# Kernel optimization log

Hardware: AMD Instinct MI355X
Metric: run time of the kernel (lower is better)

## Reference

```python
import jax, jax.numpy as jnp
import numpy as np

HEAD_DIM = 32
N_HEADS = 8
Q_DIM = 128
FF_DIM = 4 * Q_DIM
EPS = 1e-5


def layernorm(x, gamma, beta):
    mu = jnp.mean(x, axis=-1, keepdims=True)
    var = jnp.var(x, axis=-1, keepdims=True)
    return (x - mu) * jax.lax.rsqrt(var + EPS) * gamma + beta


def setup_inputs() -> dict:
    key = jax.random.key(0)
    ks = jax.random.split(key, 20)
    S, B = 1024, 16
    sc_in = 1.0 / np.sqrt(Q_DIM)
    sc_hd = 1.0 / np.sqrt(N_HEADS * HEAD_DIM)
    sc_ff = 1.0 / np.sqrt(FF_DIM)
    return {
        "sequence": jax.random.normal(ks[0], (S, B, Q_DIM), jnp.float32),
        # per-head Q/K/V projections, stacked over heads: [H, Q_dim, head_dim]
        "Wq": jax.random.uniform(ks[1], (N_HEADS, Q_DIM, HEAD_DIM), jnp.float32, -sc_in, sc_in),
        "bq": jax.random.uniform(ks[2], (N_HEADS, HEAD_DIM), jnp.float32, -sc_in, sc_in),
        "Wk": jax.random.uniform(ks[3], (N_HEADS, Q_DIM, HEAD_DIM), jnp.float32, -sc_in, sc_in),
        "bk": jax.random.uniform(ks[4], (N_HEADS, HEAD_DIM), jnp.float32, -sc_in, sc_in),
        "Wv": jax.random.uniform(ks[5], (N_HEADS, Q_DIM, HEAD_DIM), jnp.float32, -sc_in, sc_in),
        "bv": jax.random.uniform(ks[6], (N_HEADS, HEAD_DIM), jnp.float32, -sc_in, sc_in),
        # post_head_linear: [H*head_dim, Q_dim]
        "Wo": jax.random.uniform(ks[7], (N_HEADS * HEAD_DIM, Q_DIM), jnp.float32, -sc_hd, sc_hd),
        "bo": jax.random.uniform(ks[8], (Q_DIM,), jnp.float32, -sc_hd, sc_hd),
        # norm1 (note: original reuses norm1 for both layernorms)
        "gamma1": jnp.ones((Q_DIM,), jnp.float32),
        "beta1": jnp.zeros((Q_DIM,), jnp.float32),
        # FFN: Q_dim -> 4Q -> 4Q -> Q_dim
        "W1": jax.random.uniform(ks[9], (Q_DIM, FF_DIM), jnp.float32, -sc_in, sc_in),
        "b1": jax.random.uniform(ks[10], (FF_DIM,), jnp.float32, -sc_in, sc_in),
        "W2": jax.random.uniform(ks[11], (FF_DIM, FF_DIM), jnp.float32, -sc_ff, sc_ff),
        "b2": jax.random.uniform(ks[12], (FF_DIM,), jnp.float32, -sc_ff, sc_ff),
        "W3": jax.random.uniform(ks[13], (FF_DIM, Q_DIM), jnp.float32, -sc_ff, sc_ff),
        "b3": jax.random.uniform(ks[14], (Q_DIM,), jnp.float32, -sc_ff, sc_ff),
    }


def reference(sequence, Wq, bq, Wk, bk, Wv, bv, Wo, bo, gamma1, beta1, W1, b1, W2, b2, W3, b3):
    # sequence: [S, B, Q_dim] -> batch-first [B, S, Q_dim]
    x = jnp.transpose(sequence, (1, 0, 2))
    # batched per-head projections: [B, H, S, d]
    q = jnp.einsum('bsq,hqd->bhsd', x, Wq) + bq[None, :, None, :]
    k = jnp.einsum('bsq,hqd->bhsd', x, Wk) + bk[None, :, None, :]
    v = jnp.einsum('bsq,hqd->bhsd', x, Wv) + bv[None, :, None, :]
    scores = jnp.einsum('bhsd,bhtd->bhst', q, k) / np.sqrt(HEAD_DIM)
    attn = jax.nn.softmax(scores, axis=-1)
    o = jnp.einsum('bhst,bhtd->bhsd', attn, v)  # [B, H, S, d]
    B, H, S, d = o.shape
    o = jnp.transpose(o, (0, 2, 1, 3)).reshape(B, S, H * d)  # concat heads
    att_outs = o @ Wo + bo
    att_outs = layernorm(x + att_outs, gamma1, beta1)
    h = jax.nn.relu(att_outs @ W1 + b1)
    h = jax.nn.relu(h @ W2 + b2)
    h = h @ W3 + b3
    out = layernorm(att_outs + h, gamma1, beta1)  # original reuses norm1
    return jnp.transpose(out, (1, 0, 2))  # back to [S, B, Q_dim]
```

## Files before the change

kernel.cpp:

```cpp
#include <hip/hip_runtime.h>
#include <hip/hip_bf16.h>

#define S_LEN 1024
#define BATCH 16
#define QD 128
#define NH 8
#define HD 32
#define FF 512
#define NROWS (BATCH * S_LEN)
#define EPS 1e-5f

typedef __attribute__((ext_vector_type(4))) float f32x4;
typedef __attribute__((ext_vector_type(8))) short s16x8;
typedef __attribute__((ext_vector_type(4))) short s16x4;

__device__ __forceinline__ ushort f2bfu(float f) {
    union { float f; unsigned u; } v; v.f = f;
    unsigned r = (v.u + 0x7FFFu + ((v.u >> 16) & 1u)) >> 16;
    return (ushort)r;
}

__device__ __forceinline__ float bf2f(ushort u) {
    union { unsigned u; float f; } v; v.u = ((unsigned)u) << 16;
    return v.f;
}

__device__ __forceinline__ float exp2_fast(float x) {
#if __has_builtin(__builtin_amdgcn_exp2f)
    return __builtin_amdgcn_exp2f(x);
#else
    float r;
    asm("v_exp_f32 %0, %1" : "=v"(r) : "v"(x));
    return r;
#endif
}

__device__ __forceinline__ unsigned pk_bf16(float a, float b) {
    union { __hip_bfloat162 h; unsigned u; } c;
    c.h = __float22bfloat162_rn(make_float2(a, b));
    return c.u;
}

static __device__ __forceinline__ f32x4 mfma16(s16x4 a, s16x4 b, f32x4 c) {
#if __has_builtin(__builtin_amdgcn_mfma_f32_16x16x16bf16_1k)
    return __builtin_amdgcn_mfma_f32_16x16x16bf16_1k(a, b, c, 0, 0, 0);
#else
    asm volatile("v_mfma_f32_16x16x16_bf16 %0, %1, %2, %0" : "+v"(c) : "v"(a), "v"(b));
    return c;
#endif
}

static __device__ __forceinline__ f32x4 mfma32(s16x8 a, s16x8 b, f32x4 c) {
    return __builtin_amdgcn_mfma_f32_16x16x32_bf16(a, b, c, 0, 0, 0);
}

__device__ __forceinline__ void gl_lds16(const void* g, void* l) {
    __builtin_amdgcn_global_load_lds(
        (const __attribute__((address_space(1))) void*)g,
        (__attribute__((address_space(3))) void*)l, 16, 0, 0);
}

template <int K>
__device__ __forceinline__ void gemm_core(
    const ushort* __restrict__ act, const ushort* __restrict__ WTp,
    char* lds, int tok0, f32x4 acc[8]) {
    const int tid = threadIdx.x;
    const int w = tid >> 6, lane = tid & 63;
    const int qi = lane & 15, g = lane >> 4;
    const int r8 = tid >> 3;
    const int csw = (tid & 7) ^ (r8 & 7);
    const int wave_base = w * 1024;
    constexpr int NT = K / 64;

    auto STAGE = [&](int b, int ks) {
        char* buf = lds + b * 24576;
#pragma unroll
        for (int i = 0; i < 4; ++i)
            gl_lds16(WTp + (size_t)(i * 32 + r8) * K + ks + csw * 8,
                     buf + i * 4096 + wave_base);
#pragma unroll
        for (int j = 0; j < 2; ++j)
            gl_lds16(act + (size_t)(tok0 + j * 32 + r8) * K + ks + csw * 8,
                     buf + 16384 + j * 4096 + wave_base);
    };

    STAGE(0, 0);
    int cur = 0;
#pragma unroll 1
    for (int t = 0; t < NT; ++t) {
        if (t < NT - 1) {
            STAGE(cur ^ 1, (t + 1) * 64);
            asm volatile("s_waitcnt vmcnt(6)" ::: "memory");
        } else {
            asm volatile("s_waitcnt vmcnt(0)" ::: "memory");
        }
        __builtin_amdgcn_sched_barrier(0);
        __builtin_amdgcn_s_barrier();
        __builtin_amdgcn_sched_barrier(0);
        const char* A = lds + cur * 24576;
        const char* B = A + 16384;
        const int brow = w * 16 + qi;
        __builtin_amdgcn_s_setprio(1);
#pragma unroll
        for (int kk2 = 0; kk2 < 2; ++kk2) {
            s16x8 bfrag = *(const s16x8*)(B + brow * 128 +
                                          (((kk2 * 4 + g) ^ (brow & 7)) * 16));
#pragma unroll
            for (int f = 0; f < 8; ++f) {
                const int row = qi + 16 * f;
                s16x8 afrag = *(const s16x8*)(A + row * 128 +
                                              (((kk2 * 4 + g) ^ (row & 7)) * 16));
                acc[f] = mfma32(afrag, bfrag, acc[f]);
            }
        }
        __builtin_amdgcn_s_setprio(0);
        __builtin_amdgcn_sched_barrier(0);
        __builtin_amdgcn_s_barrier();
        __builtin_amdgcn_sched_barrier(0);
        cur ^= 1;
    }
}

template <int K>
__device__ __forceinline__ void gemm_core2(
    const ushort* __restrict__ act, const ushort* __restrict__ WTp,
    char* lds, int tok0, f32x4 accA[8], f32x4 accB[8]) {
    const int tid = threadIdx.x;
    const int w = tid >> 6, lane = tid & 63;
    const int qi = lane & 15, g = lane >> 4;
    const int r8 = tid >> 3;
    const int csw = (tid & 7) ^ (r8 & 7);
    const int wave_base = w * 1024;
    constexpr int NT = K / 64;

    auto STAGE = [&](int b, int ks) {
        char* buf = lds + b * 32768;
#pragma unroll
        for (int i = 0; i < 4; ++i)
            gl_lds16(WTp + (size_t)(i * 32 + r8) * K + ks + csw * 8,
                     buf + i * 4096 + wave_base);
#pragma unroll
        for (int j = 0; j < 4; ++j)
            gl_lds16(act + (size_t)(tok0 + j * 32 + r8) * K + ks + csw * 8,
                     buf + 16384 + j * 4096 + wave_base);
    };

    STAGE(0, 0);
    int cur = 0;
#pragma unroll 1
    for (int t = 0; t < NT; ++t) {
        if (t < NT - 1) {
            STAGE(cur ^ 1, (t + 1) * 64);
            asm volatile("s_waitcnt vmcnt(8)" ::: "memory");
        } else {
            asm volatile("s_waitcnt vmcnt(0)" ::: "memory");
        }
        __builtin_amdgcn_sched_barrier(0);
        __builtin_amdgcn_s_barrier();
        __builtin_amdgcn_sched_barrier(0);
        const char* A = lds + cur * 32768;
        const char* Bq = A + 16384;
        const int brow0 = w * 32 + qi;
        const int brow1 = brow0 + 16;
        __builtin_amdgcn_s_setprio(1);
#pragma unroll
        for (int kk2 = 0; kk2 < 2; ++kk2) {
            s16x8 bf0 = *(const s16x8*)(Bq + brow0 * 128 +
                                        (((kk2 * 4 + g) ^ (brow0 & 7)) * 16));
            s16x8 bf1 = *(const s16x8*)(Bq + brow1 * 128 +
                                        (((kk2 * 4 + g) ^ (brow0 & 7)) * 16));
#pragma unroll
            for (int f = 0; f < 8; ++f) {
                const int row = qi + 16 * f;
                s16x8 afrag = *(const s16x8*)(A + row * 128 +
                                              (((kk2 * 4 + g) ^ (row & 7)) * 16));
                accA[f] = mfma32(afrag, bf0, accA[f]);
                accB[f] = mfma32(afrag, bf1, accB[f]);
            }
        }
        __builtin_amdgcn_s_setprio(0);
        __builtin_amdgcn_sched_barrier(0);
        __builtin_amdgcn_s_barrier();
        __builtin_amdgcn_sched_barrier(0);
        cur ^= 1;
    }
}

__global__ __launch_bounds__(256) void prep_all(
    const float* __restrict__ seq, ushort* __restrict__ x_bf,
    const float* __restrict__ Wo, const float* __restrict__ W1,
    const float* __restrict__ W2, const float* __restrict__ W3,
    const float* __restrict__ Wq, const float* __restrict__ Wk,
    const float* __restrict__ Wv,
    ushort* __restrict__ WoT, ushort* __restrict__ W1T,
    ushort* __restrict__ W2T, ushort* __restrict__ W3T,
    ushort* __restrict__ WqkvT) {
    if (blockIdx.x < 2048) {
        int t = blockIdx.x * 256 + threadIdx.x;
        int e4 = t * 4;
        int s = e4 >> 11, b = (e4 >> 7) & 15, c = e4 & 127;
        float4 v = *(const float4*)(seq + e4);
        ushort4 o = {f2bfu(v.x), f2bfu(v.y), f2bfu(v.z), f2bfu(v.w)};
        *(ushort4*)(x_bf + ((size_t)(b * 1024 + s)) * 128 + c) = o;
        return;
    }
    int idx = (blockIdx.x - 2048) * 256 + threadIdx.x;
    if (idx < 32768) {
        int n = idx >> 8, k = idx & 255;
        WoT[n * 256 + k] = f2bfu(Wo[k * 128 + n]);
    } else if (idx < 98304) {
        int i = idx - 32768; int n = i >> 7, k = i & 127;
        W1T[n * 128 + k] = f2bfu(W1[k * 512 + n]);
    } else if (idx < 360448) {
        int i = idx - 98304; int n = i >> 9, k = i & 511;
        W2T[n * 512 + k] = f2bfu(W2[k * 512 + n]);
    } else if (idx < 425984) {
        int i = idx - 360448; int n = i >> 9, k = i & 511;
        W3T[n * 512 + k] = f2bfu(W3[k * 128 + n]);
    } else {
        int i = idx - 425984;
        int n = i >> 7, k = i & 127;
        int p = n >> 8, h = (n >> 5) & 7, d = n & 31;
        const float* W = (p == 0) ? Wq : (p == 1) ? Wk : Wv;
        WqkvT[n * 128 + k] = f2bfu(W[(h * QD + k) * HD + d]);
    }
}

__global__ __launch_bounds__(256) void qkv_mfma(
    const ushort* __restrict__ x_bf, const ushort* __restrict__ WqkvT,
    const float* __restrict__ bq, const float* __restrict__ bk,
    const float* __restrict__ bv,
    ushort* __restrict__ q_bf, ushort* __restrict__ k_bf,
    ushort* __restrict__ vT) {
    __shared__ __align__(16) char lds[2 * 32768];
    const int lane = threadIdx.x & 63;
    const int w = threadIdx.x >> 6;
    const int qi = lane & 15, g = lane >> 4;
    const int tok0 = blockIdx.x * 128;
    const int n0 = blockIdx.y * 128;

    f32x4 accA[8], accB[8];
#pragma unroll
    for (int f = 0; f < 8; ++f) {
        accA[f] = (f32x4){0.f, 0.f, 0.f, 0.f};
        accB[f] = (f32x4){0.f, 0.f, 0.f, 0.f};
    }
    gemm_core2<128>(x_bf, WqkvT + (size_t)n0 * 128, lds, tok0, accA, accB);

    const float SCALE = 0.25503491f;
#define QKV_EPI(ACC, TOK)                                                      \
    do {                                                                       \
        const int b_ = (TOK) >> 10, s_ = (TOK) & 1023;                         \
        if (n0 < 256) {                                                        \
            _Pragma("unroll") for (int f = 0; f < 8; ++f) {                    \
                int n = n0 + 16 * f + 4 * g;                                   \
                int h = (n >> 5) & 7, d = n & 31;                              \
                ushort4 pv = {f2bfu((ACC[f][0] + bq[h * 32 + d + 0]) * SCALE), \
                              f2bfu((ACC[f][1] + bq[h * 32 + d + 1]) * SCALE), \
                              f2bfu((ACC[f][2] + bq[h * 32 + d + 2]) * SCALE), \
                              f2bfu((ACC[f][3] + bq[h * 32 + d + 3]) * SCALE)};\
                *(ushort4*)(q_bf + ((size_t)(b_ * 8 + h) * 1024 + s_) * 32 + d) = pv; \
            }                                                                  \
        } else if (n0 < 512) {                                                 \
            _Pragma("unroll") for (int f = 0; f < 8; ++f) {                    \
                int n = n0 + 16 * f + 4 * g;                                   \
                int h = (n >> 5) & 7, d = n & 31;                              \
                ushort4 pv = {f2bfu(ACC[f][0] + bk[h * 32 + d + 0]),           \
                              f2bfu(ACC[f][1] + bk[h * 32 + d + 1]),           \
                              f2bfu(ACC[f][2] + bk[h * 32 + d + 2]),           \
                              f2bfu(ACC[f][3] + bk[h * 32 + d + 3])};          \
                *(ushort4*)(k_bf + ((size_t)(b_ * 8 + h) * 1024 + s_) * 32 + d) = pv; \
            }                                                                  \
        } else {                                                               \
            _Pragma("unroll") for (int f = 0; f < 8; ++f)                      \
                _Pragma("unroll") for (int r = 0; r < 4; ++r) {                \
                    int n = n0 + 16 * f + 4 * g + r;                           \
                    int h = (n >> 5) & 7, d = n & 31;                          \
                    vT[((size_t)(b_ * 8 + h) * 32 + d) * 1024 + s_] =          \
                        f2bfu(ACC[f][r] + bv[h * 32 + d]);                     \
                }                                                              \
        }                                                                      \
    } while (0)

    const int tokA = tok0 + w * 32 + qi;
    const int tokB = tokA + 16;
    QKV_EPI(accA, tokA);
    QKV_EPI(accB, tokB);
#undef QKV_EPI
}

__global__ __launch_bounds__(512) void attn_mfma(
    const ushort* __restrict__ qb, const ushort* __restrict__ kb,
    const ushort* __restrict__ vtb, ushort* __restrict__ o_bf) {
    __shared__ __align__(16) char lds[4][8192];
    const int tid = threadIdx.x;
    const int w = tid >> 6, lane = tid & 63;
    const int g = lane >> 4, qi = lane & 15;
    const int bid = blockIdx.x;
    const int swz = (bid & 7) * 128 + (bid >> 3);
    const int bh = swz >> 3;
    const int qtile = (swz & 7) * 8 + w;

    const ushort* Kb = kb + (size_t)bh * S_LEN * HD;
    const ushort* VTb = vtb + (size_t)bh * HD * S_LEN;
    const s16x8 qf = *(const s16x8*)(qb + ((size_t)bh * S_LEN + qtile * 16 + qi) * HD + g * 8);

    const int krow = 16 * w + (lane >> 2);
    const int ksrc = (lane & 3) ^ ((lane >> 3) & 3);
    const int wv = w & 3;
    const int vrow = 8 * wv + (lane >> 3);
    const int vsrc = (lane & 7) ^ ((4 * wv + (lane >> 4)) & 7);

#define STAGE(bufp, k0)                                                        \
    do {                                                                       \
        if (w < 4)                                                             \
            gl_lds16(Kb + (size_t)((k0) + krow) * HD + ksrc * 8,               \
                     (bufp) + w * 1024);                                       \
        else                                                                   \
            gl_lds16(VTb + (size_t)vrow * S_LEN + (k0) + vsrc * 8,             \
                     (bufp) + 4096 + wv * 1024);                               \
    } while (0)

    f32x4 ot0 = {0.f, 0.f, 0.f, 0.f};
    f32x4 ot1 = {0.f, 0.f, 0.f, 0.f};
    float m_run = -1e30f, l_run = 0.f;
    const f32x4 zero = {0.f, 0.f, 0.f, 0.f};

    const int koff = (g ^ ((qi >> 1) & 3)) * 16;
    const int vs = (qi >> 1) & 7;

    STAGE(lds[0], 0);
    STAGE(lds[1], 64);
    STAGE(lds[2], 128);
#pragma unroll 1
    for (int t = 0; t < 16; ++t) {
        if (t <= 13)
            asm volatile("s_waitcnt vmcnt(2)" ::: "memory");
        else if (t == 14)
            asm volatile("s_waitcnt vmcnt(1)" ::: "memory");
        else
            asm volatile("s_waitcnt vmcnt(0)" ::: "memory");
        __builtin_amdgcn_sched_barrier(0);
        __builtin_amdgcn_s_barrier();
        __builtin_amdgcn_sched_barrier(0);
        if (t <= 12) STAGE(lds[(t + 3) & 3], (t + 3) * 64);

        const char* kl = lds[t & 3];
        const char* vl = kl + 4096;
        s16x8 ka[4];
#pragma unroll
        for (int kt = 0; kt < 4; ++kt)
            ka[kt] = *(const s16x8*)(kl + (16 * kt + qi) * 64 + koff);
        s16x4 va[2][4];
#pragma unroll
        for (int h = 0; h < 2; ++h)
#pragma unroll
            for (int kt = 0; kt < 4; ++kt) {
                int c8 = 4 * kt + g;
                va[h][kt] = *(const s16x4*)(vl + (16 * h + qi) * 128 +
                                            (((c8 >> 1) ^ vs) * 16) + (c8 & 1) * 8);
            }

        f32x4 st[4];
        __builtin_amdgcn_s_setprio(1);
#pragma unroll
        for (int kt = 0; kt < 4; ++kt) st[kt] = mfma32(ka[kt], qf, zero);
        __builtin_amdgcn_s_setprio(0);

        float a0 = fmaxf(fmaxf(st[0][0], st[0][1]), fmaxf(st[0][2], st[0][3]));
        float a1 = fmaxf(fmaxf(st[1][0], st[1][1]), fmaxf(st[1][2], st[1][3]));
        float a2 = fmaxf(fmaxf(st[2][0], st[2][1]), fmaxf(st[2][2], st[2][3]));
        float a3 = fmaxf(fmaxf(st[3][0], st[3][1]), fmaxf(st[3][2], st[3][3]));
        float pmax = fmaxf(fmaxf(a0, a1), fmaxf(a2, a3));

        if (!__all(pmax <= m_run + 8.0f)) {
            float mt = pmax;
            mt = fmaxf(mt, __shfl_xor(mt, 16, 64));
            mt = fmaxf(mt, __shfl_xor(mt, 32, 64));
            float m_new = fmaxf(m_run, mt);
            float alpha = exp2_fast(m_run - m_new);
            l_run *= alpha;
#pragma unroll
            for (int r = 0; r < 4; ++r) { ot0[r] *= alpha; ot1[r] *= alpha; }
            m_run = m_new;
        }

        float p[4][4];
#pragma unroll
        for (int kt = 0; kt < 4; ++kt)
#pragma unroll
            for (int r = 0; r < 4; ++r) p[kt][r] = exp2_fast(st[kt][r] - m_run);
        float s0 = (p[0][0] + p[0][1]) + (p[0][2] + p[0][3]);
        float s1 = (p[1][0] + p[1][1]) + (p[1][2] + p[1][3]);
        float s2 = (p[2][0] + p[2][1]) + (p[2][2] + p[2][3]);
        float s3 = (p[3][0] + p[3][1]) + (p[3][2] + p[3][3]);
        l_run += (s0 + s1) + (s2 + s3);

        union { s16x4 v; uint2 u; } pb[4];
#pragma unroll
        for (int kt = 0; kt < 4; ++kt) {
            pb[kt].u.x = pk_bf16(p[kt][0], p[kt][1]);
            pb[kt].u.y = pk_bf16(p[kt][2], p[kt][3]);
        }
        __builtin_amdgcn_s_setprio(1);
#pragma unroll
        for (int kt = 0; kt < 4; ++kt) {
            ot0 = mfma16(va[0][kt], pb[kt].v, ot0);
            ot1 = mfma16(va[1][kt], pb[kt].v, ot1);
        }
        __builtin_amdgcn_s_setprio(0);
    }
#undef STAGE

    l_run += __shfl_xor(l_run, 16, 64);
    l_run += __shfl_xor(l_run, 32, 64);
    const float inv_l = 1.0f / l_run;
    const int b = bh >> 3, head = bh & 7;
    const int qg = qtile * 16 + qi;
    ushort* orow = o_bf + ((size_t)(b * S_LEN + qg)) * (NH * HD) + head * HD;
    ushort4 ob0 = {f2bfu(ot0[0] * inv_l), f2bfu(ot0[1] * inv_l),
                   f2bfu(ot0[2] * inv_l), f2bfu(ot0[3] * inv_l)};
    ushort4 ob1 = {f2bfu(ot1[0] * inv_l), f2bfu(ot1[1] * inv_l),
                   f2bfu(ot1[2] * inv_l), f2bfu(ot1[3] * inv_l)};
    *(ushort4*)(orow + g * 4) = ob0;
    *(ushort4*)(orow + 16 + g * 4) = ob1;
}

__global__ __launch_bounds__(256) void wo_ln_mfma(
    const ushort* __restrict__ o_bf, const ushort* __restrict__ WoT,
    const float* __restrict__ bo, const float* __restrict__ seq,
    const float* __restrict__ gamma, const float* __restrict__ beta,
    ushort* __restrict__ att_bf) {
    __shared__ __align__(16) char lds[2 * 24576];
    const int lane = threadIdx.x & 63;
    const int w = threadIdx.x >> 6;
    const int qi = lane & 15, g = lane >> 4;
    const int tok0 = blockIdx.x * 64;
    const int tok = tok0 + w * 16 + qi;

    f32x4 acc[8];
#pragma unroll
    for (int f = 0; f < 8; ++f) acc[f] = (f32x4){0.f, 0.f, 0.f, 0.f};
    gemm_core<256>(o_bf, WoT, lds, tok0, acc);

    const int b = tok >> 10, s = tok & 1023;
    const float* xrow = seq + (size_t)(s * BATCH + b) * QD;
    float sum = 0.f, sumsq = 0.f;
#pragma unroll
    for (int f = 0; f < 8; ++f) {
        const int c = 16 * f + 4 * g;
        float4 bv = *(const float4*)(bo + c);
        float4 xv = *(const float4*)(xrow + c);
        acc[f][0] += bv.x + xv.x;
        acc[f][1] += bv.y + xv.y;
        acc[f][2] += bv.z + xv.z;
        acc[f][3] += bv.w + xv.w;
#pragma unroll
        for (int r = 0; r < 4; ++r) { sum += acc[f][r]; sumsq += acc[f][r] * acc[f][r]; }
    }
    sum += __shfl_xor(sum, 16, 64);
    sum += __shfl_xor(sum, 32, 64);
    sumsq += __shfl_xor(sumsq, 16, 64);
    sumsq += __shfl_xor(sumsq, 32, 64);
    const float mu = sum * (1.0f / QD);
    const float var = sumsq * (1.0f / QD) - mu * mu;
    const float rstd = rsqrtf(var + EPS);

#pragma unroll
    for (int f = 0; f < 8; ++f) {
        const int c = 16 * f + 4 * g;
        float4 gm = *(const float4*)(gamma + c);
        float4 bt = *(const float4*)(beta + c);
        ushort4 pv;
        pv.x = f2bfu((acc[f][0] - mu) * rstd * gm.x + bt.x);
        pv.y = f2bfu((acc[f][1] - mu) * rstd * gm.y + bt.y);
        pv.z = f2bfu((acc[f][2] - mu) * rstd * gm.z + bt.z);
        pv.w = f2bfu((acc[f][3] - mu) * rstd * gm.w + bt.w);
        *(ushort4*)(att_bf + (size_t)tok * QD + c) = pv;
    }
}

template <int K>
__global__ __launch_bounds__(256) void ffn_mfma(
    const ushort* __restrict__ act, const ushort* __restrict__ WT,
    const float* __restrict__ bias, ushort* __restrict__ out, int N) {
    __shared__ __align__(16) char lds[2 * 32768];
    const int lane = threadIdx.x & 63;
    const int w = threadIdx.x >> 6;
    const int qi = lane & 15, g = lane >> 4;
    const int tok0 = blockIdx.x * 128;
    const int n0 = blockIdx.y * 128;

    f32x4 accA[8], accB[8];
#pragma unroll
    for (int f = 0; f < 8; ++f) {
        accA[f] = (f32x4){0.f, 0.f, 0.f, 0.f};
        accB[f] = (f32x4){0.f, 0.f, 0.f, 0.f};
    }
    gemm_core2<K>(act, WT + (size_t)n0 * K, lds, tok0, accA, accB);

    const int tokA = tok0 + w * 32 + qi;
    const int tokB = tokA + 16;
#pragma unroll
    for (int f = 0; f < 8; ++f) {
        const int c = n0 + 16 * f + 4 * g;
        float4 bv = *(const float4*)(bias + c);
        ushort4 pa, pb;
        pa.x = f2bfu(fmaxf(accA[f][0] + bv.x, 0.f));
        pa.y = f2bfu(fmaxf(accA[f][1] + bv.y, 0.f));
        pa.z = f2bfu(fmaxf(accA[f][2] + bv.z, 0.f));
        pa.w = f2bfu(fmaxf(accA[f][3] + bv.w, 0.f));
        pb.x = f2bfu(fmaxf(accB[f][0] + bv.x, 0.f));
        pb.y = f2bfu(fmaxf(accB[f][1] + bv.y, 0.f));
        pb.z = f2bfu(fmaxf(accB[f][2] + bv.z, 0.f));
        pb.w = f2bfu(fmaxf(accB[f][3] + bv.w, 0.f));
        *(ushort4*)(out + (size_t)tokA * N + c) = pa;
        *(ushort4*)(out + (size_t)tokB * N + c) = pb;
    }
}

__global__ __launch_bounds__(256) void w3_ln_mfma(
    const ushort* __restrict__ h2, const ushort* __restrict__ W3T,
    const float* __restrict__ b3, const ushort* __restrict__ att_bf,
    const float* __restrict__ gamma, const float* __restrict__ beta,
    float* __restrict__ out) {
    __shared__ __align__(16) char lds[2 * 24576];
    const int lane = threadIdx.x & 63;
    const int w = threadIdx.x >> 6;
    const int qi = lane & 15, g = lane >> 4;
    const int tok0 = blockIdx.x * 64;
    const int tok = tok0 + w * 16 + qi;

    f32x4 acc[8];
#pragma unroll
    for (int f = 0; f < 8; ++f) acc[f] = (f32x4){0.f, 0.f, 0.f, 0.f};
    gemm_core<512>(h2, W3T, lds, tok0, acc);

    float sum = 0.f, sumsq = 0.f;
#pragma unroll
    for (int f = 0; f < 8; ++f) {
        const int c = 16 * f + 4 * g;
        float4 bv = *(const float4*)(b3 + c);
        ushort4 xv = *(const ushort4*)(att_bf + (size_t)tok * QD + c);
        acc[f][0] += bv.x + bf2f(xv.x);
        acc[f][1] += bv.y + bf2f(xv.y);
        acc[f][2] += bv.z + bf2f(xv.z);
        acc[f][3] += bv.w + bf2f(xv.w);
#pragma unroll
        for (int r = 0; r < 4; ++r) { sum += acc[f][r]; sumsq += acc[f][r] * acc[f][r]; }
    }
    sum += __shfl_xor(sum, 16, 64);
    sum += __shfl_xor(sum, 32, 64);
    sumsq += __shfl_xor(sumsq, 16, 64);
    sumsq += __shfl_xor(sumsq, 32, 64);
    const float mu = sum * (1.0f / QD);
    const float var = sumsq * (1.0f / QD) - mu * mu;
    const float rstd = rsqrtf(var + EPS);

    const int b = tok >> 10, s = tok & 1023;
    float* orow = out + (size_t)(s * BATCH + b) * QD;
#pragma unroll
    for (int f = 0; f < 8; ++f) {
        const int c = 16 * f + 4 * g;
        float4 gm = *(const float4*)(gamma + c);
        float4 bt = *(const float4*)(beta + c);
        float4 ov;
        ov.x = (acc[f][0] - mu) * rstd * gm.x + bt.x;
        ov.y = (acc[f][1] - mu) * rstd * gm.y + bt.y;
        ov.z = (acc[f][2] - mu) * rstd * gm.z + bt.z;
        ov.w = (acc[f][3] - mu) * rstd * gm.w + bt.w;
        *(float4*)(orow + c) = ov;
    }
}

extern "C" void kernel_launch(void* const* d_in, const int* in_sizes, int n_in,
                              void* d_out, int out_size, void* d_ws, size_t ws_size,
                              hipStream_t stream) {
    const float* seq = (const float*)d_in[0];
    const float* Wq = (const float*)d_in[1];
    const float* bq = (const float*)d_in[2];
    const float* Wk = (const float*)d_in[3];
    const float* bk = (const float*)d_in[4];
    const float* Wv = (const float*)d_in[5];
    const float* bv = (const float*)d_in[6];
    const float* Wo = (const float*)d_in[7];
    const float* bo = (const float*)d_in[8];
    const float* gamma = (const float*)d_in[9];
    const float* beta = (const float*)d_in[10];
    const float* W1 = (const float*)d_in[11];
    const float* b1 = (const float*)d_in[12];
    const float* W2 = (const float*)d_in[13];
    const float* b2 = (const float*)d_in[14];
    const float* W3 = (const float*)d_in[15];
    const float* b3 = (const float*)d_in[16];

    char* wsb = (char*)d_ws;
    ushort* q_bf  = (ushort*)(wsb);
    ushort* k_bf  = (ushort*)(wsb + (8ull << 20));
    ushort* vT    = (ushort*)(wsb + (16ull << 20));
    ushort* o_bf  = (ushort*)(wsb + (24ull << 20));
    ushort* att_bf= (ushort*)(wsb + (40ull << 20));
    ushort* h1_bf = (ushort*)(wsb);
    ushort* h2_bf = (ushort*)(wsb + (16ull << 20));
    ushort* x_bf  = (ushort*)(wsb + (45ull << 20));
    ushort* WoT   = (ushort*)(wsb + (49ull << 20));
    ushort* W1T   = WoT + 32768;
    ushort* W2T   = W1T + 65536;
    ushort* W3T   = W2T + 262144;
    ushort* WqkvT = W3T + 65536;
    float* out = (float*)d_out;

    prep_all<<<4096, 256, 0, stream>>>(seq, x_bf, Wo, W1, W2, W3, Wq, Wk, Wv,
                                       WoT, W1T, W2T, W3T, WqkvT);
    qkv_mfma<<<dim3(NROWS / 128, 6), 256, 0, stream>>>(x_bf, WqkvT, bq, bk, bv,
                                                       q_bf, k_bf, vT);
    attn_mfma<<<1024, 512, 0, stream>>>(q_bf, k_bf, vT, o_bf);
    wo_ln_mfma<<<NROWS / 64, 256, 0, stream>>>(o_bf, WoT, bo, seq, gamma, beta, att_bf);
    ffn_mfma<QD><<<dim3(NROWS / 128, 4), 256, 0, stream>>>(att_bf, W1T, b1, h1_bf, FF);
    ffn_mfma<FF><<<dim3(NROWS / 128, 4), 256, 0, stream>>>(h1_bf, W2T, b2, h2_bf, FF);
    w3_ln_mfma<<<NROWS / 64, 256, 0, stream>>>(h2_bf, W3T, b3, att_bf, gamma, beta, out);
}
```

Before: 104.5 us.

## Process two query tiles per wave in attention to reuse staged K/V

Each wave in the attention kernel now handles two 16-row query tiles instead of one, so a block covers 256 queries and the grid is halved. Each K/V tile staged into LDS and loaded into registers is reused for twice as many queries, cutting global and LDS traffic per query. In exchange, register pressure rises, there are fewer blocks to hide latency, and each block runs a longer serial loop.

```diff
diff --git a/kernel.cpp b/kernel.cpp
--- a/kernel.cpp
+++ b/kernel.cpp
@@ -297,13 +297,15 @@
     const int w = tid >> 6, lane = tid & 63;
     const int g = lane >> 4, qi = lane & 15;
     const int bid = blockIdx.x;
-    const int swz = (bid & 7) * 128 + (bid >> 3);
-    const int bh = swz >> 3;
-    const int qtile = (swz & 7) * 8 + w;
+    const int swz = (bid & 7) * 64 + (bid >> 3);
+    const int bh = swz >> 2;
+    const int q0 = (swz & 3) * 256 + w * 32;
 
     const ushort* Kb = kb + (size_t)bh * S_LEN * HD;
     const ushort* VTb = vtb + (size_t)bh * HD * S_LEN;
-    const s16x8 qf = *(const s16x8*)(qb + ((size_t)bh * S_LEN + qtile * 16 + qi) * HD + g * 8);
+    const ushort* Qp = qb + ((size_t)bh * S_LEN + q0 + qi) * HD + g * 8;
+    const s16x8 qf0 = *(const s16x8*)(Qp);
+    const s16x8 qf1 = *(const s16x8*)(Qp + 16 * HD);
 
     const int krow = 16 * w + (lane >> 2);
     const int ksrc = (lane & 3) ^ ((lane >> 3) & 3);
@@ -321,9 +323,12 @@
                      (bufp) + 4096 + wv * 1024);                               \
     } while (0)
 
-    f32x4 ot0 = {0.f, 0.f, 0.f, 0.f};
-    f32x4 ot1 = {0.f, 0.f, 0.f, 0.f};
-    float m_run = -1e30f, l_run = 0.f;
+    f32x4 ot[2][2];
+#pragma unroll
+    for (int qa = 0; qa < 2; ++qa)
+#pragma unroll
+        for (int h = 0; h < 2; ++h) ot[qa][h] = (f32x4){0.f, 0.f, 0.f, 0.f};
+    float m_run[2] = {-1e30f, -1e30f}, l_run[2] = {0.f, 0.f};
     const f32x4 zero = {0.f, 0.f, 0.f, 0.f};
 
     const int koff = (g ^ ((qi >> 1) & 3)) * 16;
@@ -361,69 +366,81 @@
                                             (((c8 >> 1) ^ vs) * 16) + (c8 & 1) * 8);
             }
 
-        f32x4 st[4];
-        __builtin_amdgcn_s_setprio(1);
-#pragma unroll
-        for (int kt = 0; kt < 4; ++kt) st[kt] = mfma32(ka[kt], qf, zero);
-        __builtin_amdgcn_s_setprio(0);
-
-        float a0 = fmaxf(fmaxf(st[0][0], st[0][1]), fmaxf(st[0][2], st[0][3]));
-        float a1 = fmaxf(fmaxf(st[1][0], st[1][1]), fmaxf(st[1][2], st[1][3]));
-        float a2 = fmaxf(fmaxf(st[2][0], st[2][1]), fmaxf(st[2][2], st[2][3]));
-        float a3 = fmaxf(fmaxf(st[3][0], st[3][1]), fmaxf(st[3][2], st[3][3]));
-        float pmax = fmaxf(fmaxf(a0, a1), fmaxf(a2, a3));
-
-        if (!__all(pmax <= m_run + 8.0f)) {
-            float mt = pmax;
-            mt = fmaxf(mt, __shfl_xor(mt, 16, 64));
-            mt = fmaxf(mt, __shfl_xor(mt, 32, 64));
-            float m_new = fmaxf(m_run, mt);
-            float alpha = exp2_fast(m_run - m_new);
-            l_run *= alpha;
-#pragma unroll
-            for (int r = 0; r < 4; ++r) { ot0[r] *= alpha; ot1[r] *= alpha; }
-            m_run = m_new;
+#pragma unroll
+        for (int qa = 0; qa < 2; ++qa) {
+            const s16x8 qf = qa ? qf1 : qf0;
+            f32x4 st[4];
+            __builtin_amdgcn_s_setprio(1);
+#pragma unroll
+            for (int kt = 0; kt < 4; ++kt) st[kt] = mfma32(ka[kt], qf, zero);
+            __builtin_amdgcn_s_setprio(0);
+
+            float a0 = fmaxf(fmaxf(st[0][0], st[0][1]), fmaxf(st[0][2], st[0][3]));
+            float a1 = fmaxf(fmaxf(st[1][0], st[1][1]), fmaxf(st[1][2], st[1][3]));
+            float a2 = fmaxf(fmaxf(st[2][0], st[2][1]), fmaxf(st[2][2], st[2][3]));
+            float a3 = fmaxf(fmaxf(st[3][0], st[3][1]), fmaxf(st[3][2], st[3][3]));
+            float pmax = fmaxf(fmaxf(a0, a1), fmaxf(a2, a3));
+
+            if (!__all(pmax <= m_run[qa] + 8.0f)) {
+                float mt = pmax;
+                mt = fmaxf(mt, __shfl_xor(mt, 16, 64));
+                mt = fmaxf(mt, __shfl_xor(mt, 32, 64));
+                float m_new = fmaxf(m_run[qa], mt);
+                float alpha = exp2_fast(m_run[qa] - m_new);
+                l_run[qa] *= alpha;
+#pragma unroll
+                for (int r = 0; r < 4; ++r) {
+                    ot[qa][0][r] *= alpha;
+                    ot[qa][1][r] *= alpha;
+                }
+                m_run[qa] = m_new;
+            }
+
+            float p[4][4];
+#pragma unroll
+            for (int kt = 0; kt < 4; ++kt)
+#pragma unroll
+                for (int r = 0; r < 4; ++r)
+                    p[kt][r] = exp2_fast(st[kt][r] - m_run[qa]);
+            float s0 = (p[0][0] + p[0][1]) + (p[0][2] + p[0][3]);
+            float s1 = (p[1][0] + p[1][1]) + (p[1][2] + p[1][3]);
+            float s2 = (p[2][0] + p[2][1]) + (p[2][2] + p[2][3]);
+            float s3 = (p[3][0] + p[3][1]) + (p[3][2] + p[3][3]);
+            l_run[qa] += (s0 + s1) + (s2 + s3);
+
+            union { s16x4 v; uint2 u; } pb[4];
+#pragma unroll
+            for (int kt = 0; kt < 4; ++kt) {
+                pb[kt].u.x = pk_bf16(p[kt][0], p[kt][1]);
+                pb[kt].u.y = pk_bf16(p[kt][2], p[kt][3]);
+            }
+            __builtin_amdgcn_s_setprio(1);
+#pragma unroll
+            for (int kt = 0; kt < 4; ++kt) {
+                ot[qa][0] = mfma16(va[0][kt], pb[kt].v, ot[qa][0]);
+                ot[qa][1] = mfma16(va[1][kt], pb[kt].v, ot[qa][1]);
+            }
+            __builtin_amdgcn_s_setprio(0);
         }
-
-        float p[4][4];
-#pragma unroll
-        for (int kt = 0; kt < 4; ++kt)
-#pragma unroll
-            for (int r = 0; r < 4; ++r) p[kt][r] = exp2_fast(st[kt][r] - m_run);
-        float s0 = (p[0][0] + p[0][1]) + (p[0][2] + p[0][3]);
-        float s1 = (p[1][0] + p[1][1]) + (p[1][2] + p[1][3]);
-        float s2 = (p[2][0] + p[2][1]) + (p[2][2] + p[2][3]);
-        float s3 = (p[3][0] + p[3][1]) + (p[3][2] + p[3][3]);
-        l_run += (s0 + s1) + (s2 + s3);
-
-        union { s16x4 v; uint2 u; } pb[4];
-#pragma unroll
-        for (int kt = 0; kt < 4; ++kt) {
-            pb[kt].u.x = pk_bf16(p[kt][0], p[kt][1]);
-            pb[kt].u.y = pk_bf16(p[kt][2], p[kt][3]);
-        }
-        __builtin_amdgcn_s_setprio(1);
-#pragma unroll
-        for (int kt = 0; kt < 4; ++kt) {
-            ot0 = mfma16(va[0][kt], pb[kt].v, ot0);
-            ot1 = mfma16(va[1][kt], pb[kt].v, ot1);
-        }
-        __builtin_amdgcn_s_setprio(0);
     }
 #undef STAGE
 
-    l_run += __shfl_xor(l_run, 16, 64);
-    l_run += __shfl_xor(l_run, 32, 64);
-    const float inv_l = 1.0f / l_run;
     const int b = bh >> 3, head = bh & 7;
-    const int qg = qtile * 16 + qi;
-    ushort* orow = o_bf + ((size_t)(b * S_LEN + qg)) * (NH * HD) + head * HD;
-    ushort4 ob0 = {f2bfu(ot0[0] * inv_l), f2bfu(ot0[1] * inv_l),
-                   f2bfu(ot0[2] * inv_l), f2bfu(ot0[3] * inv_l)};
-    ushort4 ob1 = {f2bfu(ot1[0] * inv_l), f2bfu(ot1[1] * inv_l),
-                   f2bfu(ot1[2] * inv_l), f2bfu(ot1[3] * inv_l)};
-    *(ushort4*)(orow + g * 4) = ob0;
-    *(ushort4*)(orow + 16 + g * 4) = ob1;
+#pragma unroll
+    for (int qa = 0; qa < 2; ++qa) {
+        float l = l_run[qa];
+        l += __shfl_xor(l, 16, 64);
+        l += __shfl_xor(l, 32, 64);
+        const float inv_l = 1.0f / l;
+        const int q = q0 + qa * 16 + qi;
+        ushort* orow = o_bf + ((size_t)(b * S_LEN + q)) * (NH * HD) + head * HD;
+        ushort4 ob0 = {f2bfu(ot[qa][0][0] * inv_l), f2bfu(ot[qa][0][1] * inv_l),
+                       f2bfu(ot[qa][0][2] * inv_l), f2bfu(ot[qa][0][3] * inv_l)};
+        ushort4 ob1 = {f2bfu(ot[qa][1][0] * inv_l), f2bfu(ot[qa][1][1] * inv_l),
+                       f2bfu(ot[qa][1][2] * inv_l), f2bfu(ot[qa][1][3] * inv_l)};
+        *(ushort4*)(orow + g * 4) = ob0;
+        *(ushort4*)(orow + 16 + g * 4) = ob1;
+    }
 }
 
 __global__ __launch_bounds__(256) void wo_ln_mfma(
@@ -614,7 +631,7 @@
                                        WoT, W1T, W2T, W3T, WqkvT);
     qkv_mfma<<<dim3(NROWS / 128, 6), 256, 0, stream>>>(x_bf, WqkvT, bq, bk, bv,
                                                        q_bf, k_bf, vT);
-    attn_mfma<<<1024, 512, 0, stream>>>(q_bf, k_bf, vT, o_bf);
+    attn_mfma<<<512, 512, 0, stream>>>(q_bf, k_bf, vT, o_bf);
     wo_ln_mfma<<<NROWS / 64, 256, 0, stream>>>(o_bf, WoT, bo, seq, gamma, beta, att_bf);
     ffn_mfma<QD><<<dim3(NROWS / 128, 4), 256, 0, stream>>>(att_bf, W1T, b1, h1_bf, FF);
     ffn_mfma<FF><<<dim3(NROWS / 128, 4), 256, 0, stream>>>(h1_bf, W2T, b2, h2_bf, FF);
```

Result: no change. 104.7 us (+0.2%).
